# Kernel tuning notes

Measured on AMD Instinct MI355X. Metric: run time of the kernel, lower is better.

## Reference

```python
import jax, jax.numpy as jnp
import numpy as np

V, NSEG, MAXLEN, D, H = 32000, 2, 512, 768, 12
HS = D // H  # head_size = 64
B, T, NMASK = 16, 512, 20
LN_EPS = 1e-5


def setup_inputs() -> dict:
    key = jax.random.key(0)
    ks = jax.random.split(key, 16)
    s = 0.02
    return {
        "sequence": jax.random.randint(ks[0], (B, T), 0, V),
        "segment": jax.random.randint(ks[1], (B, T), 0, NSEG),
        "attn_mask": jax.random.randint(ks[2], (B, T), 0, 2).astype(jnp.int32),
        "masked_pos": jax.random.randint(ks[3], (B, NMASK), 0, T),
        "tok_emb": jax.random.normal(ks[4], (V, D), jnp.float32) * s,
        "seg_emb": jax.random.normal(ks[5], (NSEG, D), jnp.float32) * s,
        "pos_emb": jax.random.normal(ks[6], (MAXLEN, D), jnp.float32) * s,
        "ln_g": jnp.ones((D,), jnp.float32),
        "ln_b": jnp.zeros((D,), jnp.float32),
        "Wq": jax.random.normal(ks[7], (H, D, HS), jnp.float32) * s,
        "Wk": jax.random.normal(ks[8], (H, D, HS), jnp.float32) * s,
        "Wv": jax.random.normal(ks[9], (H, D, HS), jnp.float32) * s,
        "W_lm": jax.random.normal(ks[10], (D, V), jnp.float32) * s,
        "b_lm": jnp.zeros((V,), jnp.float32),
        "W_cls": jax.random.normal(ks[11], (D, 2), jnp.float32) * s,
        "b_cls": jnp.zeros((2,), jnp.float32),
    }


def reference(sequence, segment, attn_mask, masked_pos,
              tok_emb, seg_emb, pos_emb, ln_g, ln_b,
              Wq, Wk, Wv, W_lm, b_lm, W_cls, b_cls):
    Tlen = sequence.shape[1]
    # --- BERTEmbedding (dropout = identity in eval) ---
    emb = tok_emb[sequence] + seg_emb[segment] + pos_emb[jnp.arange(Tlen)][None]  # [B,T,D]
    mu = jnp.mean(emb, axis=-1, keepdims=True)
    var = jnp.mean(jnp.square(emb - mu), axis=-1, keepdims=True)
    x = (emb - mu) * jax.lax.rsqrt(var + LN_EPS) * ln_g + ln_b  # [B,T,D]

    # --- Multi-head attention (heads batched instead of Python loop) ---
    q = jnp.einsum('btd,hds->bhts', x, Wq)
    k = jnp.einsum('btd,hds->bhts', x, Wk)
    v = jnp.einsum('btd,hds->bhts', x, Wv)
    wei = jnp.einsum('bhts,bhus->bhtu', q, k) * (HS ** -0.5)  # [B,H,T,T]
    # original: wei.masked_fill(attn_mask[:, :, None] == 0, -1e-11) -> masks over query dim
    wei = jnp.where(attn_mask[:, None, :, None] == 0, jnp.float32(-1e-11), wei)
    wei = jax.nn.softmax(wei, axis=-1)
    out = jnp.einsum('bhtu,bhus->bhts', wei, v)  # [B,H,T,HS]
    x = out.transpose(0, 2, 1, 3).reshape(out.shape[0], Tlen, H * HS)  # cat heads -> [B,T,D]

    # --- Output heads ---
    x_masked = jnp.take_along_axis(x, masked_pos[:, :, None], axis=1)  # [B,NMASK,D]
    logits_lm = x_masked @ W_lm + b_lm          # [B,NMASK,V]
    logits_clsf = x[:, 0, :] @ W_cls + b_cls    # [B,2]
    return (logits_lm, logits_clsf)
```

## Files before the change

kernel.cpp:

```cpp
#include <hip/hip_runtime.h>
#include <hip/hip_bf16.h>

#define V_     32000
#define NSEG_  2
#define MAXLEN_ 512
#define D_     768
#define H_     12
#define HS_    64
#define B_     16
#define T_     512
#define NMASK_ 20
#define LN_EPS_ 1e-5f

typedef __hip_bfloat16 bf16;
typedef unsigned short ushortT;
typedef __attribute__((ext_vector_type(8))) short short8;
typedef __attribute__((ext_vector_type(4))) float f32x4;
typedef __attribute__((ext_vector_type(4))) unsigned int u32x4;
typedef __attribute__((ext_vector_type(4))) unsigned short u16x4;

__device__ __forceinline__ ushortT f2bu(float f) {
    bf16 h = __float2bfloat16(f);
    return *reinterpret_cast<ushortT*>(&h);
}

__global__ void k_embed_ln(const int* __restrict__ seq, const int* __restrict__ seg,
                           const float* __restrict__ tok, const float* __restrict__ sege,
                           const float* __restrict__ pos, const float* __restrict__ g,
                           const float* __restrict__ bb, ushortT* __restrict__ xb) {
    int row = blockIdx.x;
    int t = row & (T_ - 1);
    int tid = threadIdx.x;
    __shared__ float wsum[3], wsq[3];

    int sidx = seq[row];
    int gidx = seg[row];

    f32x4 e = *(const f32x4*)(tok  + (size_t)sidx * D_ + tid * 4);
    f32x4 e2 = *(const f32x4*)(sege + (size_t)gidx * D_ + tid * 4);
    f32x4 e3 = *(const f32x4*)(pos  + (size_t)t    * D_ + tid * 4);
    e = e + e2 + e3;

    float ls = e.x + e.y + e.z + e.w;
    float lq = e.x * e.x + e.y * e.y + e.z * e.z + e.w * e.w;
    #pragma unroll
    for (int o = 32; o > 0; o >>= 1) {
        ls += __shfl_down(ls, o);
        lq += __shfl_down(lq, o);
    }
    if ((tid & 63) == 0) { wsum[tid >> 6] = ls; wsq[tid >> 6] = lq; }
    __syncthreads();
    float s  = wsum[0] + wsum[1] + wsum[2];
    float sq = wsq[0] + wsq[1] + wsq[2];
    float mean = s * (1.0f / D_);
    float var  = sq * (1.0f / D_) - mean * mean;
    float rstd = rsqrtf(var + LN_EPS_);

    f32x4 g4 = *(const f32x4*)(g  + tid * 4);
    f32x4 b4 = *(const f32x4*)(bb + tid * 4);
    f32x4 x4;
    x4.x = (e.x - mean) * rstd * g4.x + b4.x;
    x4.y = (e.y - mean) * rstd * g4.y + b4.y;
    x4.z = (e.z - mean) * rstd * g4.z + b4.z;
    x4.w = (e.w - mean) * rstd * g4.w + b4.w;
    u16x4 ov = {f2bu(x4.x), f2bu(x4.y), f2bu(x4.z), f2bu(x4.w)};
    *(u16x4*)(xb + (size_t)row * D_ + tid * 4) = ov;
}

__global__ void k_prep_wqkv(const float* __restrict__ Wq, const float* __restrict__ Wk,
                            const float* __restrict__ Wv, ushortT* __restrict__ Wt) {
    int blk = blockIdx.x;
    int which = blk / H_, h = blk % H_;
    int kc = blockIdx.y * 64;
    const float* W = (which == 0) ? Wq : (which == 1) ? Wk : Wv;
    __shared__ float tile[64][65];
    int tid = threadIdx.x, c = tid & 63, rgrp = tid >> 6;
    for (int kk = rgrp; kk < 64; kk += 4)
        tile[kk][c] = W[((size_t)h * D_ + kc + kk) * HS_ + c];
    __syncthreads();
    for (int ss = rgrp; ss < 64; ss += 4)
        Wt[((size_t)which * D_ + h * HS_ + ss) * D_ + kc + c] = f2bu(tile[c][ss]);
}

__global__ void k_gather_xm(const float* __restrict__ x2, const int* __restrict__ masked_pos,
                            ushortT* __restrict__ xm) {
    int r = blockIdx.x;
    int tid = threadIdx.x;
    if (r < B_ * NMASK_) {
        int b = r / NMASK_, m = r % NMASK_;
        int t = masked_pos[b * NMASK_ + m];
        for (int d = tid; d < D_; d += 256)
            xm[(size_t)r * D_ + d] = f2bu(x2[((size_t)b * T_ + t) * D_ + d]);
    } else {
        for (int d = tid; d < D_; d += 256)
            xm[(size_t)r * D_ + d] = 0;
    }
}

__device__ __forceinline__ void stage_chunk(const ushortT* __restrict__ src, int row_stride,
                                            int r0, int k0, ushortT* dst, int w, int lane) {
    #pragma unroll
    for (int i = 0; i < 2; ++i) {
        int slot = w * 64 + lane + i * 256;
        int row = slot >> 2;
        int cs = ((slot & 3) ^ (row & 3)) * 8;
        __builtin_amdgcn_global_load_lds(
            (const __attribute__((address_space(1))) void*)(src + (size_t)(r0 + row) * row_stride + k0 + cs),
            (__attribute__((address_space(3))) void*)(dst + (w * 64 + i * 256) * 8),
            16, 0, 0);
    }
}

__device__ __forceinline__ void gemm128_2ph(const ushortT* __restrict__ A,
                                            const ushortT* __restrict__ Bt,
                                            int m0, int n0,
                                            ushortT* lds,
                                            f32x4 acc[4][4]) {
    const int NT = D_ / 32;
    int tid = threadIdx.x;
    int lane = tid & 63, w = tid >> 6;
    int wr = (w >> 1) * 64, wc = (w & 1) * 64;
    int l16 = lane & 15, lk = lane >> 4;
    int sw = (lk ^ (l16 & 3)) * 8;

    #pragma unroll
    for (int i = 0; i < 4; ++i)
        #pragma unroll
        for (int j = 0; j < 4; ++j)
            acc[i][j] = (f32x4){0.f, 0.f, 0.f, 0.f};

    stage_chunk(A, D_, m0, 0, lds, w, lane);
    stage_chunk(Bt, D_, n0, 0, lds + 4096, w, lane);
    asm volatile("s_waitcnt vmcnt(0)" ::: "memory");
    __builtin_amdgcn_s_barrier();

    for (int t = 0; t < NT; ++t) {
        int cur = (t & 1) * 8192;
        int nxt = 8192 - cur;
        if (t + 1 < NT) {
            stage_chunk(A, D_, m0, (t + 1) * 32, lds + nxt, w, lane);
            stage_chunk(Bt, D_, n0, (t + 1) * 32, lds + nxt + 4096, w, lane);
        }

        const ushortT* Asc = lds + cur;
        const ushortT* Bsc = lds + cur + 4096;
        short8 a[4], bfr[4];
        #pragma unroll
        for (int i = 0; i < 4; ++i) {
            a[i]   = *(const short8*)(Asc + (wr + i * 16 + l16) * 32 + sw);
            bfr[i] = *(const short8*)(Bsc + (wc + i * 16 + l16) * 32 + sw);
        }
        #pragma unroll
        for (int i = 0; i < 4; ++i)
            #pragma unroll
            for (int j = 0; j < 4; ++j)
                acc[i][j] = __builtin_amdgcn_mfma_f32_16x16x32_bf16(a[i], bfr[j], acc[i][j], 0, 0, 0);

        asm volatile("s_waitcnt vmcnt(0)" ::: "memory");
        __builtin_amdgcn_s_barrier();
    }
}

__global__ __launch_bounds__(256, 4)
void k_gemm_qkv(const ushortT* __restrict__ xb, const ushortT* __restrict__ WcatT,
                ushortT* __restrict__ qb, ushortT* __restrict__ kb,
                ushortT* __restrict__ vb) {
    __shared__ ushortT lds[128 * 136];
    f32x4 acc[4][4];
    int lin = (blockIdx.x & 7) * 144 + (blockIdx.x >> 3);
    int n0 = (lin % 18) * 128, m0 = (lin / 18) * 128;
    gemm128_2ph(xb, WcatT, m0, n0, lds, acc);

    int tid = threadIdx.x;
    int lane = tid & 63, w = tid >> 6;
    int wr = (w >> 1) * 64, wc = (w & 1) * 64;
    int l16 = lane & 15, lk = lane >> 4;

    #pragma unroll
    for (int j = 0; j < 4; ++j) {
        int n = wc + j * 16 + l16;
        #pragma unroll
        for (int i = 0; i < 4; ++i) {
            #pragma unroll
            for (int r = 0; r < 4; ++r) {
                int m = wr + i * 16 + lk * 4 + r;
                lds[m * 136 + n] = f2bu(acc[i][j][r]);
            }
        }
    }
    __syncthreads();

    int which = n0 / D_;
    int nrem0 = n0 - which * D_;
    ushortT* outp = (which == 0) ? qb : (which == 1) ? kb : vb;
    int b = m0 >> 9;
    int t0 = m0 & (T_ - 1);
    #pragma unroll
    for (int p = 0; p < 8; ++p) {
        int chunk = p * 256 + tid;
        int row = chunk >> 4;
        int nc = (chunk & 15) * 8;
        int h = (nrem0 >> 6) + (nc >> 6);
        int s0 = nc & 63;
        u32x4 v = *(const u32x4*)(&lds[row * 136 + nc]);
        *(u32x4*)(outp + ((size_t)(b * H_ + h) * T_ + (t0 + row)) * HS_ + s0) = v;
    }
}

__global__ __launch_bounds__(256, 6)
void k_gemm_lm(const ushortT* __restrict__ xm, const float* __restrict__ Wlm,
               const float* __restrict__ blm, float* __restrict__ out) {
    const int NT = D_ / 32;
    __shared__ ushortT As[2][4096];
    __shared__ ushortT Bs[2][64 * 36];
    f32x4 acc[4][2];

    int bid = blockIdx.x;
    const int q = 187, r = 4;
    int xcd = bid & 7, idx = bid >> 3;
    int lin = (xcd < r) ? xcd * (q + 1) + idx : r * (q + 1) + (xcd - r) * q + idx;
    int nt = lin / 3, mt = lin - nt * 3;
    int m0 = mt * 128, n0 = nt * 64;

    int tid = threadIdx.x;
    int lane = tid & 63, w = tid >> 6;
    int wr = (w >> 1) * 64, wc = (w & 1) * 32;
    int l16 = lane & 15, lk = lane >> 4;
    int sw = (lk ^ (l16 & 3)) * 8;
    int n_l = tid & 63;
    int kr  = tid >> 6;

    #pragma unroll
    for (int i = 0; i < 4; ++i)
        #pragma unroll
        for (int j = 0; j < 2; ++j)
            acc[i][j] = (f32x4){0.f, 0.f, 0.f, 0.f};

    const float* Wbase = Wlm + n0 + n_l;

    float bw[8];
    stage_chunk(xm, D_, m0, 0, As[0], w, lane);
    #pragma unroll
    for (int g = 0; g < 8; ++g)
        bw[g] = Wbase[(size_t)(kr * 8 + g) * V_];
    asm volatile("s_waitcnt vmcnt(0)" ::: "memory");
    #pragma unroll
    for (int c = 0; c < 2; ++c) {
        u16x4 pk = {f2bu(bw[c * 4]), f2bu(bw[c * 4 + 1]), f2bu(bw[c * 4 + 2]), f2bu(bw[c * 4 + 3])};
        *(u16x4*)(&Bs[0][n_l * 36 + kr * 8 + c * 4]) = pk;
    }
    asm volatile("s_waitcnt lgkmcnt(0)" ::: "memory");
    __builtin_amdgcn_s_barrier();

    for (int t = 0; t < NT; ++t) {
        int cur = t & 1, nx = cur ^ 1;
        if (t + 1 < NT) {
            stage_chunk(xm, D_, m0, (t + 1) * 32, As[nx], w, lane);
            int k0 = (t + 1) * 32;
            #pragma unroll
            for (int g = 0; g < 8; ++g)
                bw[g] = Wbase[(size_t)(k0 + kr * 8 + g) * V_];
        }

        short8 a[4], bfr[2];
        #pragma unroll
        for (int i = 0; i < 4; ++i)
            a[i] = *(const short8*)(&As[cur][(wr + i * 16 + l16) * 32 + sw]);
        #pragma unroll
        for (int j = 0; j < 2; ++j)
            bfr[j] = *(const short8*)(&Bs[cur][(wc + j * 16 + l16) * 36 + lk * 8]);
        #pragma unroll
        for (int i = 0; i < 4; ++i)
            #pragma unroll
            for (int j = 0; j < 2; ++j)
                acc[i][j] = __builtin_amdgcn_mfma_f32_16x16x32_bf16(a[i], bfr[j], acc[i][j], 0, 0, 0);

        if (t + 1 < NT) {
            #pragma unroll
            for (int c = 0; c < 2; ++c) {
                u16x4 pk = {f2bu(bw[c * 4]), f2bu(bw[c * 4 + 1]), f2bu(bw[c * 4 + 2]), f2bu(bw[c * 4 + 3])};
                *(u16x4*)(&Bs[nx][n_l * 36 + kr * 8 + c * 4]) = pk;
            }
        }
        asm volatile("s_waitcnt vmcnt(0) lgkmcnt(0)" ::: "memory");
        __builtin_amdgcn_s_barrier();
    }

    #pragma unroll
    for (int j = 0; j < 2; ++j) {
        int n = n0 + wc + j * 16 + l16;
        float bias = blm[n];
        #pragma unroll
        for (int i = 0; i < 4; ++i) {
            #pragma unroll
            for (int r2 = 0; r2 < 4; ++r2) {
                int m = m0 + wr + i * 16 + lk * 4 + r2;
                if (m < B_ * NMASK_)
                    out[(size_t)m * V_ + n] = acc[i][j][r2] + bias;
            }
        }
    }
}

__global__ __launch_bounds__(256, 4)
void k_attn_mfma(const ushortT* __restrict__ qb, const ushortT* __restrict__ kb,
                 const ushortT* __restrict__ vb, const int* __restrict__ attn_mask,
                 float* __restrict__ x2) {
    int lin = (blockIdx.x & 7) * 192 + (blockIdx.x >> 3);
    int qt = lin & 7, bh = lin >> 3;
    int b = bh / H_, h = bh % H_;
    int tid = threadIdx.x, lane = tid & 63, w = tid >> 6;
    int l16 = lane & 15, lk = lane >> 4;

    __shared__ ushortT QP[64][72];
    __shared__ ushortT Ks[64][72];
    __shared__ ushortT Vts[64][72];
    __shared__ float mskS[64];

    const ushortT* Qg = qb + ((size_t)bh * T_ + qt * 64) * HS_;
    #pragma unroll
    for (int i = 0; i < 2; ++i) {
        int slot = tid + i * 256;
        int r = slot >> 3, c8 = (slot & 7) * 8;
        *(u32x4*)(&QP[r][c8]) = *(const u32x4*)(Qg + (size_t)r * HS_ + c8);
    }
    if (tid < 64)
        mskS[tid] = attn_mask[b * T_ + qt * 64 + tid] ? 0.125f : 0.0f;
    __syncthreads();

    short8 aq[2];
    #pragma unroll
    for (int ks = 0; ks < 2; ++ks)
        aq[ks] = *(const short8*)(&QP[w * 16 + l16][ks * 32 + lk * 8]);
    float mrow[4];
    #pragma unroll
    for (int r = 0; r < 4; ++r)
        mrow[r] = mskS[w * 16 + lk * 4 + r];

    float lsum[4];
    f32x4 accO[4];
    #pragma unroll
    for (int r = 0; r < 4; ++r) lsum[r] = 0.f;
    #pragma unroll
    for (int j = 0; j < 4; ++j)
        accO[j] = (f32x4){0.f, 0.f, 0.f, 0.f};

    for (int kt = 0; kt < 8; ++kt) {
        __syncthreads();
        {
            int r = tid >> 2, c = (tid & 3) * 16;
            const ushortT* Kg = kb + ((size_t)bh * T_ + kt * 64 + r) * HS_ + c;
            *(u32x4*)(&Ks[r][c])     = *(const u32x4*)(Kg);
            *(u32x4*)(&Ks[r][c + 8]) = *(const u32x4*)(Kg + 8);
        }
        {
            int r = lane;
            int c = w * 16;
            const ushortT* Vg = vb + ((size_t)bh * T_ + kt * 64 + r) * HS_ + c;
            short8 v0 = *(const short8*)(Vg);
            short8 v1 = *(const short8*)(Vg + 8);
            #pragma unroll
            for (int e = 0; e < 8; ++e) Vts[c + e][r]     = (ushortT)v0[e];
            #pragma unroll
            for (int e = 0; e < 8; ++e) Vts[c + 8 + e][r] = (ushortT)v1[e];
        }
        __syncthreads();

        f32x4 accS[4];
        #pragma unroll
        for (int j = 0; j < 4; ++j)
            accS[j] = (f32x4){0.f, 0.f, 0.f, 0.f};
        #pragma unroll
        for (int ks = 0; ks < 2; ++ks) {
            short8 bk[4];
            #pragma unroll
            for (int j = 0; j < 4; ++j)
                bk[j] = *(const short8*)(&Ks[j * 16 + l16][ks * 32 + lk * 8]);
            #pragma unroll
            for (int j = 0; j < 4; ++j)
                accS[j] = __builtin_amdgcn_mfma_f32_16x16x32_bf16(aq[ks], bk[j], accS[j], 0, 0, 0);
        }

        #pragma unroll
        for (int r = 0; r < 4; ++r) {
            int rowl = lk * 4 + r;
            float m = mrow[r];
            float p0 = __expf(accS[0][r] * m);
            float p1 = __expf(accS[1][r] * m);
            float p2 = __expf(accS[2][r] * m);
            float p3 = __expf(accS[3][r] * m);
            lsum[r] += (p0 + p1) + (p2 + p3);
            QP[w * 16 + rowl][0 * 16 + l16] = f2bu(p0);
            QP[w * 16 + rowl][1 * 16 + l16] = f2bu(p1);
            QP[w * 16 + rowl][2 * 16 + l16] = f2bu(p2);
            QP[w * 16 + rowl][3 * 16 + l16] = f2bu(p3);
        }

        #pragma unroll
        for (int ks2 = 0; ks2 < 2; ++ks2) {
            short8 ap = *(const short8*)(&QP[w * 16 + l16][ks2 * 32 + lk * 8]);
            short8 bv[4];
            #pragma unroll
            for (int j = 0; j < 4; ++j)
                bv[j] = *(const short8*)(&Vts[j * 16 + l16][ks2 * 32 + lk * 8]);
            #pragma unroll
            for (int j = 0; j < 4; ++j)
                accO[j] = __builtin_amdgcn_mfma_f32_16x16x32_bf16(ap, bv[j], accO[j], 0, 0, 0);
        }
    }

    #pragma unroll
    for (int r = 0; r < 4; ++r) {
        float s = lsum[r];
        #pragma unroll
        for (int off = 1; off < 16; off <<= 1)
            s += __shfl_xor(s, off);
        float inv = 1.0f / s;
        int t = qt * 64 + w * 16 + lk * 4 + r;
        float* outp = x2 + ((size_t)b * T_ + t) * D_ + h * HS_;
        #pragma unroll
        for (int j = 0; j < 4; ++j)
            outp[j * 16 + l16] = accO[j][r] * inv;
    }
}

__global__ void k_cls(const float* __restrict__ x2, const float* __restrict__ Wc,
                      const float* __restrict__ bc, float* __restrict__ out) {
    int b = blockIdx.x;
    int tid = threadIdx.x;
    __shared__ float red0[4], red1[4];
    float a0 = 0.f, a1 = 0.f;
    const float* xr = x2 + (size_t)b * T_ * D_;
    for (int d = tid; d < D_; d += 256) {
        float x = xr[d];
        a0 += x * Wc[d * 2];
        a1 += x * Wc[d * 2 + 1];
    }
    #pragma unroll
    for (int o = 32; o > 0; o >>= 1) {
        a0 += __shfl_down(a0, o);
        a1 += __shfl_down(a1, o);
    }
    if ((tid & 63) == 0) { red0[tid >> 6] = a0; red1[tid >> 6] = a1; }
    __syncthreads();
    if (tid == 0)
        out[b * 2]     = red0[0] + red0[1] + red0[2] + red0[3] + bc[0];
    if (tid == 1)
        out[b * 2 + 1] = red1[0] + red1[1] + red1[2] + red1[3] + bc[1];
}

extern "C" void kernel_launch(void* const* d_in, const int* in_sizes, int n_in,
                              void* d_out, int out_size, void* d_ws, size_t ws_size,
                              hipStream_t stream) {
    const int* seq        = (const int*)d_in[0];
    const int* seg        = (const int*)d_in[1];
    const int* attn_mask  = (const int*)d_in[2];
    const int* masked_pos = (const int*)d_in[3];
    const float* tok  = (const float*)d_in[4];
    const float* sege = (const float*)d_in[5];
    const float* pos  = (const float*)d_in[6];
    const float* ln_g = (const float*)d_in[7];
    const float* ln_b = (const float*)d_in[8];
    const float* Wq   = (const float*)d_in[9];
    const float* Wk   = (const float*)d_in[10];
    const float* Wv   = (const float*)d_in[11];
    const float* Wlm  = (const float*)d_in[12];
    const float* blm  = (const float*)d_in[13];
    const float* Wc   = (const float*)d_in[14];
    const float* bc   = (const float*)d_in[15];

    float* out_lm  = (float*)d_out;
    float* out_cls = out_lm + (size_t)B_ * NMASK_ * V_;

    const size_t XSZ = (size_t)B_ * T_ * D_;
    float* ws = (float*)d_ws;
    float*   x2   = ws;
    ushortT* base = (ushortT*)(ws + XSZ);
    ushortT* xb    = base;
    ushortT* qb    = base + XSZ;
    ushortT* kb    = base + 2 * XSZ;
    ushortT* vb    = base + 3 * XSZ;
    ushortT* WcatT = base + 4 * XSZ;
    ushortT* xm    = base;

    k_embed_ln<<<B_ * T_, 192, 0, stream>>>(seq, seg, tok, sege, pos, ln_g, ln_b, xb);
    k_prep_wqkv<<<dim3(3 * H_, 12), 256, 0, stream>>>(Wq, Wk, Wv, WcatT);
    k_gemm_qkv<<<1152, 256, 0, stream>>>(xb, WcatT, qb, kb, vb);
    k_attn_mfma<<<192 * 8, 256, 0, stream>>>(qb, kb, vb, attn_mask, x2);
    k_gather_xm<<<384, 256, 0, stream>>>(x2, masked_pos, xm);
    k_gemm_lm<<<1500, 256, 0, stream>>>(xm, Wlm, blm, out_lm);
    k_cls<<<B_, 256, 0, stream>>>(x2, Wc, bc, out_cls);
}
```

Before: 152.9 us.

## Cover all 384 padded LM rows per block so W_lm is read once

The LM-head GEMM previously split M (320 rows padded to 384) into three 128-row tiles, so each 64-column slice of the fp32 W_lm was loaded and converted to bf16 three times across blocks. Each block now stages all 384 rows of xm and computes a 384x64 tile, with each wave handling 96 rows across all 64 columns, so W_lm (about 98 MB in fp32) is streamed from memory only once. The price is a larger LDS footprint, more accumulator registers (occupancy bound lowered to 2), and a third as many blocks (500), which reduces parallelism for latency hiding.

```diff
diff --git a/kernel.cpp b/kernel.cpp
--- a/kernel.cpp
+++ b/kernel.cpp
@@ -111,6 +111,20 @@
     }
 }
 
+__device__ __forceinline__ void stage_chunk384(const ushortT* __restrict__ src,
+                                               int k0, ushortT* dst, int w, int lane) {
+    #pragma unroll
+    for (int i = 0; i < 6; ++i) {
+        int slot = w * 64 + lane + i * 256;
+        int row = slot >> 2;
+        int cs = ((slot & 3) ^ (row & 3)) * 8;
+        __builtin_amdgcn_global_load_lds(
+            (const __attribute__((address_space(1))) void*)(src + (size_t)row * D_ + k0 + cs),
+            (__attribute__((address_space(3))) void*)(dst + (w * 64 + i * 256) * 8),
+            16, 0, 0);
+    }
+}
+
 __device__ __forceinline__ void gemm128_2ph(const ushortT* __restrict__ A,
                                             const ushortT* __restrict__ Bt,
                                             int m0, int n0,
@@ -207,39 +221,38 @@
     }
 }
 
-__global__ __launch_bounds__(256, 6)
+__global__ __launch_bounds__(256, 2)
 void k_gemm_lm(const ushortT* __restrict__ xm, const float* __restrict__ Wlm,
                const float* __restrict__ blm, float* __restrict__ out) {
     const int NT = D_ / 32;
-    __shared__ ushortT As[2][4096];
+    __shared__ ushortT As[2][12288];
     __shared__ ushortT Bs[2][64 * 36];
-    f32x4 acc[4][2];
+    f32x4 acc[6][4];
 
     int bid = blockIdx.x;
-    const int q = 187, r = 4;
+    const int q = 62, r = 4;
     int xcd = bid & 7, idx = bid >> 3;
-    int lin = (xcd < r) ? xcd * (q + 1) + idx : r * (q + 1) + (xcd - r) * q + idx;
-    int nt = lin / 3, mt = lin - nt * 3;
-    int m0 = mt * 128, n0 = nt * 64;
+    int nt = (xcd < r) ? xcd * (q + 1) + idx : r * (q + 1) + (xcd - r) * q + idx;
+    int n0 = nt * 64;
 
     int tid = threadIdx.x;
     int lane = tid & 63, w = tid >> 6;
-    int wr = (w >> 1) * 64, wc = (w & 1) * 32;
+    int wr = w * 96;
     int l16 = lane & 15, lk = lane >> 4;
     int sw = (lk ^ (l16 & 3)) * 8;
     int n_l = tid & 63;
     int kr  = tid >> 6;
 
     #pragma unroll
-    for (int i = 0; i < 4; ++i)
-        #pragma unroll
-        for (int j = 0; j < 2; ++j)
+    for (int i = 0; i < 6; ++i)
+        #pragma unroll
+        for (int j = 0; j < 4; ++j)
             acc[i][j] = (f32x4){0.f, 0.f, 0.f, 0.f};
 
     const float* Wbase = Wlm + n0 + n_l;
 
     float bw[8];
-    stage_chunk(xm, D_, m0, 0, As[0], w, lane);
+    stage_chunk384(xm, 0, As[0], w, lane);
     #pragma unroll
     for (int g = 0; g < 8; ++g)
         bw[g] = Wbase[(size_t)(kr * 8 + g) * V_];
@@ -255,24 +268,24 @@
     for (int t = 0; t < NT; ++t) {
         int cur = t & 1, nx = cur ^ 1;
         if (t + 1 < NT) {
-            stage_chunk(xm, D_, m0, (t + 1) * 32, As[nx], w, lane);
+            stage_chunk384(xm, (t + 1) * 32, As[nx], w, lane);
             int k0 = (t + 1) * 32;
             #pragma unroll
             for (int g = 0; g < 8; ++g)
                 bw[g] = Wbase[(size_t)(k0 + kr * 8 + g) * V_];
         }
 
-        short8 a[4], bfr[2];
-        #pragma unroll
-        for (int i = 0; i < 4; ++i)
+        short8 a[6], bfr[4];
+        #pragma unroll
+        for (int i = 0; i < 6; ++i)
             a[i] = *(const short8*)(&As[cur][(wr + i * 16 + l16) * 32 + sw]);
         #pragma unroll
-        for (int j = 0; j < 2; ++j)
-            bfr[j] = *(const short8*)(&Bs[cur][(wc + j * 16 + l16) * 36 + lk * 8]);
-        #pragma unroll
-        for (int i = 0; i < 4; ++i)
-            #pragma unroll
-            for (int j = 0; j < 2; ++j)
+        for (int j = 0; j < 4; ++j)
+            bfr[j] = *(const short8*)(&Bs[cur][(j * 16 + l16) * 36 + lk * 8]);
+        #pragma unroll
+        for (int i = 0; i < 6; ++i)
+            #pragma unroll
+            for (int j = 0; j < 4; ++j)
                 acc[i][j] = __builtin_amdgcn_mfma_f32_16x16x32_bf16(a[i], bfr[j], acc[i][j], 0, 0, 0);
 
         if (t + 1 < NT) {
@@ -287,14 +300,14 @@
     }
 
     #pragma unroll
-    for (int j = 0; j < 2; ++j) {
-        int n = n0 + wc + j * 16 + l16;
+    for (int j = 0; j < 4; ++j) {
+        int n = n0 + j * 16 + l16;
         float bias = blm[n];
         #pragma unroll
-        for (int i = 0; i < 4; ++i) {
+        for (int i = 0; i < 6; ++i) {
             #pragma unroll
             for (int r2 = 0; r2 < 4; ++r2) {
-                int m = m0 + wr + i * 16 + lk * 4 + r2;
+                int m = wr + i * 16 + lk * 4 + r2;
                 if (m < B_ * NMASK_)
                     out[(size_t)m * V_ + n] = acc[i][j][r2] + bias;
             }
@@ -488,6 +501,6 @@
     k_gemm_qkv<<<1152, 256, 0, stream>>>(xb, WcatT, qb, kb, vb);
     k_attn_mfma<<<192 * 8, 256, 0, stream>>>(qb, kb, vb, attn_mask, x2);
     k_gather_xm<<<384, 256, 0, stream>>>(x2, masked_pos, xm);
-    k_gemm_lm<<<1500, 256, 0, stream>>>(xm, Wlm, blm, out_lm);
+    k_gemm_lm<<<500, 256, 0, stream>>>(xm, Wlm, blm, out_lm);
     k_cls<<<B_, 256, 0, stream>>>(x2, Wc, bc, out_cls);
 }
```

Result: no change. 154.2 us (+0.8%).
